# Kernel tuning notes

Hardware: AMD Instinct MI355X
Metric: run time of the kernel (lower is better)

## Reference

```python
import jax, jax.numpy as jnp
import numpy as np
from jax import lax

B, CIN, COUT, K, H, W = 16, 256, 256, 3, 128, 128
R = 16  # LoRA rank


def setup_inputs() -> dict:
    key = jax.random.key(0)
    ks = jax.random.split(key, 16)
    s = 0.05
    return {
        "x": jax.random.normal(ks[0], (B, CIN, H, W), jnp.float32),
        "wms": jax.random.normal(ks[1], (2, B, 32), jnp.float32),
        "conv_w": jax.random.normal(ks[2], (COUT, CIN, K, K), jnp.float32) * s,
        "conv_b": jax.random.normal(ks[3], (COUT,), jnp.float32) * s,
        "e1_w1": jax.random.normal(ks[4], (128, 32), jnp.float32) * s,
        "e1_b1": jax.random.normal(ks[5], (128,), jnp.float32) * s,
        "e1_w2": jax.random.normal(ks[6], (256, 128), jnp.float32) * s,
        "e1_b2": jax.random.normal(ks[7], (256,), jnp.float32) * s,
        "e2_w1": jax.random.normal(ks[8], (128, 32), jnp.float32) * s,
        "e2_b1": jax.random.normal(ks[9], (128,), jnp.float32) * s,
        "e2_w2": jax.random.normal(ks[10], (256, 128), jnp.float32) * s,
        "e2_b2": jax.random.normal(ks[11], (256,), jnp.float32) * s,
        "lora_A1": jax.random.normal(ks[12], (R, CIN * K), jnp.float32),
        "lora_A2": jax.random.normal(ks[13], (R, CIN * K), jnp.float32),
        "lora_B": jax.random.normal(ks[14], (COUT * K, R), jnp.float32) * s,
    }


def _embed(v, w1, b1, w2, b2):
    # Linear(32,128) -> LeakyReLU(0.2) -> Linear(128,256)
    h = v @ w1.T + b1
    h = jnp.where(h >= 0, h, 0.2 * h)
    return h @ w2.T + b2


def _conv_same(x, w):
    # NCHW conv, stride 1, padding 1
    return lax.conv_general_dilated(x, w, (1, 1), [(1, 1), (1, 1)],
                                    dimension_numbers=("NCHW", "OIHW", "NCHW"))


def reference(x, wms, conv_w, conv_b, e1_w1, e1_b1, e1_w2, e1_b2,
              e2_w1, e2_b1, e2_w2, e2_b2, lora_A1, lora_A2, lora_B):
    wm1, wm2 = wms[0], wms[1]
    coff1 = _embed(wm1, e1_w1, e1_b1, e1_w2, e1_b2).reshape(B, R, R)
    coff2 = _embed(wm2, e2_w1, e2_b1, e2_w2, e2_b2).reshape(B, R, R)

    org = _conv_same(x, conv_w) + conv_b[None, :, None, None]

    # per-sample LoRA weights: (COUT*K, R) @ (R,R) @ (R, CIN*K) -> (B, COUT, CIN, K, K)
    wA = jnp.einsum('pr,brq,qc->bpc', lora_B, coff1, lora_A1).reshape(B, COUT, CIN, K, K)
    wB = jnp.einsum('pr,brq,qc->bpc', lora_B, coff2, lora_A2).reshape(B, COUT, CIN, K, K)

    def per_sample_conv(xi, wi):
        return _conv_same(xi[None], wi)[0]

    outA = jax.vmap(per_sample_conv)(x, wA)
    outB = jax.vmap(per_sample_conv)(x, wB)
    return org + outA + outB
```

## Files before the change

### kernel.cpp

```cpp
#include <hip/hip_runtime.h>
#include <hip/hip_bf16.h>
#include <stdint.h>

typedef __bf16 bf16x8 __attribute__((ext_vector_type(8)));
typedef float f32x4 __attribute__((ext_vector_type(4)));
typedef unsigned short ushort8v __attribute__((ext_vector_type(8)));

#define NB    16
#define CIN   256
#define COUT  256
#define HH    128
#define WW    128

#define OFF_ZROW  0u
#define OFF_COFF  (1u << 16)
#define OFF_TMPS  (1u << 17)
#define OFF_WEFF  (1u << 20)
#define OFF_XT    (20u * 1024u * 1024u)
#define XT_PER_B  (128u * 128u * 256u * 2u)

__device__ inline void gload16(const void* g, void* l) {
  __builtin_amdgcn_global_load_lds(
      (const __attribute__((address_space(1))) void*)g,
      (__attribute__((address_space(3))) void*)l, 16, 0, 0);
}

__device__ inline ushort f2bf(float f) {
  __hip_bfloat16 h = __float2bfloat16(f);
  union { __hip_bfloat16 b; ushort u; } cv;
  cv.b = h;
  return cv.u;
}

__global__ void k_coff(const float* __restrict__ wms,
                       const float* __restrict__ w1a, const float* __restrict__ b1a,
                       const float* __restrict__ w2a, const float* __restrict__ b2a,
                       const float* __restrict__ w1b, const float* __restrict__ b1b,
                       const float* __restrict__ w2b, const float* __restrict__ b2b,
                       float* __restrict__ coff) {
  int br = blockIdx.x >> 4, b = blockIdx.x & 15;
  const float* w1 = br ? w1b : w1a;
  const float* b1 = br ? b1b : b1a;
  const float* w2 = br ? w2b : w2a;
  const float* b2 = br ? b2b : b2a;
  const float* v = wms + (br * 16 + b) * 32;
  __shared__ float h[128];
  int t = threadIdx.x;
  if (t < 128) {
    float a = b1[t];
#pragma unroll
    for (int i = 0; i < 32; ++i) a += w1[t * 32 + i] * v[i];
    h[t] = a >= 0.f ? a : 0.2f * a;
  }
  __syncthreads();
  float a = b2[t];
  for (int j = 0; j < 128; ++j) a += w2[t * 128 + j] * h[j];
  coff[(br * 16 + b) * 256 + t] = a;
}

__global__ void k_tmps(const float* __restrict__ coff,
                       const float* __restrict__ A1, const float* __restrict__ A2,
                       float* __restrict__ tmpS) {
  int b = blockIdx.x >> 4, r = blockIdx.x & 15;
  __shared__ float c1[16], c2[16];
  int t = threadIdx.x;
  if (t < 16) {
    c1[t] = coff[b * 256 + r * 16 + t];
    c2[t] = coff[(16 + b) * 256 + r * 16 + t];
  }
  __syncthreads();
  for (int c = t; c < 768; c += 256) {
    float s = 0.f;
#pragma unroll
    for (int q = 0; q < 16; ++q) s += c1[q] * A1[q * 768 + c] + c2[q] * A2[q * 768 + c];
    tmpS[(b * 16 + r) * 768 + c] = s;
  }
}

__global__ __launch_bounds__(256) void k_weff(const float* __restrict__ conv_w,
                                              const float* __restrict__ loraB,
                                              const float* __restrict__ tmpS,
                                              __hip_bfloat16* __restrict__ Weff) {
  int bid = blockIdx.x;
  int co = bid & 255, b = bid >> 8;
  int t = threadIdx.x;
  __shared__ float Bs[3][16];
  __shared__ ushort obuf[2304];
  if (t < 48) Bs[t >> 4][t & 15] = loraB[(co * 3 + (t >> 4)) * 16 + (t & 15)];
  __syncthreads();
  const float* T = tmpS + (size_t)b * 16 * 768;
  const float* W = conv_w + (size_t)co * 2304;
#pragma unroll
  for (int k = 0; k < 3; ++k) {
#pragma unroll
    for (int cc = 0; cc < 3; ++cc) {
      int c = cc * 256 + t;
      float s = W[k * 768 + c];
#pragma unroll
      for (int r = 0; r < 16; ++r) s += Bs[k][r] * T[r * 768 + c];
      int f = k * 768 + c;
      int ci = f / 9, tt = f - ci * 9;
      obuf[tt * 256 + ci] = f2bf(s);
    }
  }
  __syncthreads();
#pragma unroll
  for (int tt = 0; tt < 9; ++tt)
    ((ushort*)Weff)[((size_t)(b * 9 + tt) * 256 + co) * 256 + t] = obuf[tt * 256 + t];
}

__global__ __launch_bounds__(256) void k_xt(const float* __restrict__ x,
                                            __hip_bfloat16* __restrict__ xT, int b0) {
  __shared__ ushort t[32][132];
  int bid = blockIdx.x;
  int cb = bid & 7, h = (bid >> 3) & 127, bp = bid >> 10;
  int b = b0 + bp;
  int tid = threadIdx.x;
  int ci2 = tid >> 5, w4 = (tid & 31) * 4;
  const float* srcb = x + ((size_t)(b * 256 + cb * 32) * 128 + h) * 128;
#pragma unroll
  for (int k = 0; k < 4; ++k) {
    int c = ci2 + k * 8;
    float4 v = *(const float4*)(srcb + (size_t)c * 16384 + w4);
    ushort4 u;
    u.x = f2bf(v.x);
    u.y = f2bf(v.y);
    u.z = f2bf(v.z);
    u.w = f2bf(v.w);
    *(ushort4*)&t[c][w4] = u;
  }
  __syncthreads();
  int w = tid >> 1, hf = tid & 1;
  ushort8v o0, o1;
#pragma unroll
  for (int j = 0; j < 8; ++j) {
    o0[j] = t[hf * 16 + j][w];
    o1[j] = t[hf * 16 + 8 + j][w];
  }
  ushort* dst = (ushort*)xT + (size_t)bp * 128 * 128 * 256 +
                ((size_t)h * 128 + w) * 256 + cb * 32 + hf * 16;
  *(ushort8v*)dst = o0;
  *(ushort8v*)(dst + 8) = o1;
}

__global__ __launch_bounds__(512) void k_conv(
    const __hip_bfloat16* __restrict__ xT,
    const __hip_bfloat16* __restrict__ Weff,
    const __hip_bfloat16* __restrict__ zrow,
    const float* __restrict__ cbias,
    float* __restrict__ out, int b0) {
  __shared__ __align__(16) __hip_bfloat16 xs[4 * 130 * 32];
  __shared__ __align__(16) __hip_bfloat16 wbuf[3 * 256 * 32];

  int bid = blockIdx.x;
  int hp = bid & 63, bp = bid >> 6;
  int b = b0 + bp;
  int h0 = hp * 2;

  int tid = threadIdx.x;
  int wid = tid >> 6, lane = tid & 63;
  int l15 = lane & 15, lh = lane >> 4;
  int wm = wid >> 2, wn = wid & 3;
  int row = wn >> 1, w0 = (wn & 1) * 64;
  int lrow = lane >> 2;
  int sgx = (lane & 3) ^ (((1 + lrow) >> 1) & 3);
  int sgw = (lane & 3) ^ ((lrow >> 1) & 3);
  int asw = (l15 >> 1) & 3;

  if (tid < 256) {
    int ri = tid >> 6, which = (tid >> 5) & 1, ci = tid & 31;
    ((ushort*)xs)[ri * 4160 + (which ? 129 : 0) * 32 + ci] = 0;
  }

  f32x4 acc[8][4];
#pragma unroll
  for (int mf = 0; mf < 8; ++mf)
#pragma unroll
    for (int nf = 0; nf < 4; ++nf) acc[mf][nf] = (f32x4){0.f, 0.f, 0.f, 0.f};

  const __hip_bfloat16* xTb = xT + (size_t)bp * 128 * 128 * 256;

  for (int cb8 = 0; cb8 < 8; ++cb8) {
    int c0 = cb8 * 32;
    __syncthreads();

#pragma unroll
    for (int k = 0; k < 4; ++k) {
      int s = wid * 4 + k;
      int ri = s >> 3, wblk = s & 7;
      int h = h0 + ri - 1;
      const __hip_bfloat16* srow = (h >= 0 && h < 128) ? (xTb + (size_t)h * 128 * 256) : zrow;
      const __hip_bfloat16* src = srow + (wblk * 16 + lrow) * 256 + c0 + sgx * 8;
      gload16((const void*)src, (void*)(xs + ri * 4160 + (1 + wblk * 16) * 32));
    }

#pragma unroll 1
    for (int kh = 0; kh < 3; ++kh) {
      if (kh) __syncthreads();
#pragma unroll
      for (int k = 0; k < 6; ++k) {
        int s = wid * 6 + k;
        int kw = s >> 4, cblk = s & 15;
        const __hip_bfloat16* src =
            Weff + (((size_t)(b * 9 + kh * 3 + kw) * 256 + cblk * 16 + lrow) * 256 +
                    c0 + sgw * 8);
        gload16((const void*)src, (void*)(wbuf + kw * 8192 + cblk * 512));
      }
      __syncthreads();

#pragma unroll
      for (int kw = 0; kw < 3; ++kw) {
        int bsw = ((l15 + kw) >> 1) & 3;
        bf16x8 af[8], bfr[4];
#pragma unroll
        for (int mf = 0; mf < 8; ++mf)
          af[mf] = *(const bf16x8*)&wbuf[kw * 8192 + (wm * 128 + mf * 16 + l15) * 32 +
                                         ((lh ^ asw) * 8)];
#pragma unroll
        for (int nf = 0; nf < 4; ++nf)
          bfr[nf] = *(const bf16x8*)&xs[(row + kh) * 4160 +
                                        (w0 + nf * 16 + l15 + kw) * 32 + ((lh ^ bsw) * 8)];
#pragma unroll
        for (int mf = 0; mf < 8; ++mf)
#pragma unroll
          for (int nf = 0; nf < 4; ++nf)
            acc[mf][nf] = __builtin_amdgcn_mfma_f32_16x16x32_bf16(af[mf], bfr[nf], acc[mf][nf], 0, 0, 0);
      }
    }
  }

#pragma unroll
  for (int mf = 0; mf < 8; ++mf) {
    int cobase = wm * 128 + mf * 16 + lh * 4;
#pragma unroll
    for (int r = 0; r < 4; ++r) {
      int co = cobase + r;
      float bias = cbias[co];
      size_t obase = ((size_t)(b * 256 + co) * 128 + (h0 + row)) * 128 + w0 + l15;
#pragma unroll
      for (int nf = 0; nf < 4; ++nf) out[obase + nf * 16] = acc[mf][nf][r] + bias;
    }
  }
}

extern "C" void kernel_launch(void* const* d_in, const int* in_sizes, int n_in,
                              void* d_out, int out_size, void* d_ws, size_t ws_size,
                              hipStream_t stream) {
  const float* x      = (const float*)d_in[0];
  const float* wms    = (const float*)d_in[1];
  const float* conv_w = (const float*)d_in[2];
  const float* conv_b = (const float*)d_in[3];
  const float* e1w1   = (const float*)d_in[4];
  const float* e1b1   = (const float*)d_in[5];
  const float* e1w2   = (const float*)d_in[6];
  const float* e1b2   = (const float*)d_in[7];
  const float* e2w1   = (const float*)d_in[8];
  const float* e2b1   = (const float*)d_in[9];
  const float* e2w2   = (const float*)d_in[10];
  const float* e2b2   = (const float*)d_in[11];
  const float* A1     = (const float*)d_in[12];
  const float* A2     = (const float*)d_in[13];
  const float* loraB  = (const float*)d_in[14];
  float* out = (float*)d_out;

  uint8_t* ws = (uint8_t*)d_ws;
  __hip_bfloat16* zrow = (__hip_bfloat16*)(ws + OFF_ZROW);
  float* coff          = (float*)(ws + OFF_COFF);
  float* tmpS          = (float*)(ws + OFF_TMPS);
  __hip_bfloat16* Weff = (__hip_bfloat16*)(ws + OFF_WEFF);
  __hip_bfloat16* xT   = (__hip_bfloat16*)(ws + OFF_XT);

  int G = 16;
  while (G > 1 && (size_t)OFF_XT + (size_t)G * XT_PER_B > ws_size) G >>= 1;

  hipMemsetAsync(zrow, 0, 65536, stream);
  k_coff<<<32, 256, 0, stream>>>(wms, e1w1, e1b1, e1w2, e1b2, e2w1, e2b1, e2w2, e2b2, coff);
  k_tmps<<<256, 256, 0, stream>>>(coff, A1, A2, tmpS);
  k_weff<<<16 * 256, 256, 0, stream>>>(conv_w, loraB, tmpS, Weff);
  for (int g = 0; g < 16; g += G) {
    k_xt<<<G * 1024, 256, 0, stream>>>(x, xT, g);
    k_conv<<<G * 64, 512, 0, stream>>>(xT, Weff, zrow, conv_b, out, g);
  }
}
```

Before: 486.7 us.

## Double-buffer conv weight and input tiles, switch to 32x32x16 MFMA

Restructures the implicit-GEMM conv main loop. Weight slices are now loaded one tap at a time into a double buffer and the next channel block of input rows is prefetched into a second buffer, so global-to-LDS loads overlap with MFMA work instead of stalling behind a barrier. The inner product moves from 16x16x32 to 32x32x16 MFMA with a matching swizzle and epilogue, and the code adds s_setprio around the math plus a two-blocks-per-CU occupancy hint. The cost is doubled LDS for the input tile, one barrier per tap, and more register pressure under the tighter launch bound.

New measurement: 514.1 us. 5.6% more time.

```diff
diff --git a/kernel.cpp b/kernel.cpp
--- a/kernel.cpp
+++ b/kernel.cpp
@@ -3,7 +3,7 @@
 #include <stdint.h>
 
 typedef __bf16 bf16x8 __attribute__((ext_vector_type(8)));
-typedef float f32x4 __attribute__((ext_vector_type(4)));
+typedef float f32x16 __attribute__((ext_vector_type(16)));
 typedef unsigned short ushort8v __attribute__((ext_vector_type(8)));
 
 #define NB    16
@@ -143,14 +143,14 @@
   *(ushort8v*)(dst + 8) = o1;
 }
 
-__global__ __launch_bounds__(512) void k_conv(
+__global__ __launch_bounds__(512, 2) void k_conv(
     const __hip_bfloat16* __restrict__ xT,
     const __hip_bfloat16* __restrict__ Weff,
     const __hip_bfloat16* __restrict__ zrow,
     const float* __restrict__ cbias,
     float* __restrict__ out, int b0) {
-  __shared__ __align__(16) __hip_bfloat16 xs[4 * 130 * 32];
-  __shared__ __align__(16) __hip_bfloat16 wbuf[3 * 256 * 32];
+  __shared__ __align__(16) __hip_bfloat16 xs[2 * 4 * 130 * 32];
+  __shared__ __align__(16) __hip_bfloat16 wsl[2 * 256 * 32];
 
   int bid = blockIdx.x;
   int hp = bid & 63, bp = bid >> 6;
@@ -159,86 +159,133 @@
 
   int tid = threadIdx.x;
   int wid = tid >> 6, lane = tid & 63;
-  int l15 = lane & 15, lh = lane >> 4;
+  int l31 = lane & 31, gh = lane >> 5;
   int wm = wid >> 2, wn = wid & 3;
   int row = wn >> 1, w0 = (wn & 1) * 64;
   int lrow = lane >> 2;
   int sgx = (lane & 3) ^ (((1 + lrow) >> 1) & 3);
   int sgw = (lane & 3) ^ ((lrow >> 1) & 3);
-  int asw = (l15 >> 1) & 3;
-
-  if (tid < 256) {
-    int ri = tid >> 6, which = (tid >> 5) & 1, ci = tid & 31;
-    ((ushort*)xs)[ri * 4160 + (which ? 129 : 0) * 32 + ci] = 0;
-  }
-
-  f32x4 acc[8][4];
-#pragma unroll
-  for (int mf = 0; mf < 8; ++mf)
-#pragma unroll
-    for (int nf = 0; nf < 4; ++nf) acc[mf][nf] = (f32x4){0.f, 0.f, 0.f, 0.f};
+  int x2 = (l31 >> 1) & 3;
+
+  ((ushort*)xs)[(tid >> 8) * 16640 + ((tid >> 6) & 3) * 4160 +
+                (((tid >> 5) & 1) ? 129 * 32 : 0) + (tid & 31)] = 0;
 
   const __hip_bfloat16* xTb = xT + (size_t)bp * 128 * 128 * 256;
 
-  for (int cb8 = 0; cb8 < 8; ++cb8) {
-    int c0 = cb8 * 32;
-    __syncthreads();
-
+  {
+    int cblk = wid * 2;
+#pragma unroll
+    for (int k = 0; k < 2; ++k)
+      gload16(Weff + (((size_t)(b * 9 + 0) * 256 + (cblk + k) * 16 + lrow) * 256 + sgw * 8),
+              wsl + (cblk + k) * 512);
 #pragma unroll
     for (int k = 0; k < 4; ++k) {
       int s = wid * 4 + k;
       int ri = s >> 3, wblk = s & 7;
       int h = h0 + ri - 1;
       const __hip_bfloat16* srow = (h >= 0 && h < 128) ? (xTb + (size_t)h * 128 * 256) : zrow;
-      const __hip_bfloat16* src = srow + (wblk * 16 + lrow) * 256 + c0 + sgx * 8;
-      gload16((const void*)src, (void*)(xs + ri * 4160 + (1 + wblk * 16) * 32));
+      gload16(srow + (wblk * 16 + lrow) * 256 + sgx * 8,
+              xs + ri * 4160 + (1 + wblk * 16) * 32);
     }
+  }
+
+  f32x16 acc[4][2];
+#pragma unroll
+  for (int mf = 0; mf < 4; ++mf)
+#pragma unroll
+    for (int nf = 0; nf < 2; ++nf)
+#pragma unroll
+      for (int q = 0; q < 16; ++q) acc[mf][nf][q] = 0.f;
+
+  __syncthreads();
 
 #pragma unroll 1
+  for (int cb8 = 0; cb8 < 8; ++cb8) {
+    const __hip_bfloat16* xsb = xs + (cb8 & 1) * 16640;
+#pragma unroll
     for (int kh = 0; kh < 3; ++kh) {
-      if (kh) __syncthreads();
-#pragma unroll
-      for (int k = 0; k < 6; ++k) {
-        int s = wid * 6 + k;
-        int kw = s >> 4, cblk = s & 15;
-        const __hip_bfloat16* src =
-            Weff + (((size_t)(b * 9 + kh * 3 + kw) * 256 + cblk * 16 + lrow) * 256 +
-                    c0 + sgw * 8);
-        gload16((const void*)src, (void*)(wbuf + kw * 8192 + cblk * 512));
-      }
-      __syncthreads();
-
 #pragma unroll
       for (int kw = 0; kw < 3; ++kw) {
-        int bsw = ((l15 + kw) >> 1) & 3;
-        bf16x8 af[8], bfr[4];
-#pragma unroll
-        for (int mf = 0; mf < 8; ++mf)
-          af[mf] = *(const bf16x8*)&wbuf[kw * 8192 + (wm * 128 + mf * 16 + l15) * 32 +
-                                         ((lh ^ asw) * 8)];
-#pragma unroll
-        for (int nf = 0; nf < 4; ++nf)
-          bfr[nf] = *(const bf16x8*)&xs[(row + kh) * 4160 +
-                                        (w0 + nf * 16 + l15 + kw) * 32 + ((lh ^ bsw) * 8)];
-#pragma unroll
-        for (int mf = 0; mf < 8; ++mf)
-#pragma unroll
-          for (int nf = 0; nf < 4; ++nf)
-            acc[mf][nf] = __builtin_amdgcn_mfma_f32_16x16x32_bf16(af[mf], bfr[nf], acc[mf][nf], 0, 0, 0);
+        const int tap = kh * 3 + kw;
+        int cur = (cb8 ^ tap) & 1;
+        const __hip_bfloat16* wcur = wsl + cur * 8192;
+        __hip_bfloat16* wnxt = wsl + (cur ^ 1) * 8192;
+
+        if (tap < 8) {
+          int cblk = wid * 2;
+#pragma unroll
+          for (int k = 0; k < 2; ++k)
+            gload16(Weff + (((size_t)(b * 9 + tap + 1) * 256 + (cblk + k) * 16 + lrow) * 256 +
+                            cb8 * 32 + sgw * 8),
+                    wnxt + (cblk + k) * 512);
+        } else if (cb8 < 7) {
+          int cblk = wid * 2;
+#pragma unroll
+          for (int k = 0; k < 2; ++k)
+            gload16(Weff + (((size_t)(b * 9 + 0) * 256 + (cblk + k) * 16 + lrow) * 256 +
+                            (cb8 + 1) * 32 + sgw * 8),
+                    wnxt + (cblk + k) * 512);
+        }
+        if (tap == 0 && cb8 < 7) {
+          __hip_bfloat16* xnxt = xs + ((cb8 + 1) & 1) * 16640;
+          int c0n = (cb8 + 1) * 32;
+#pragma unroll
+          for (int k = 0; k < 4; ++k) {
+            int s = wid * 4 + k;
+            int ri = s >> 3, wblk = s & 7;
+            int h = h0 + ri - 1;
+            const __hip_bfloat16* srow = (h >= 0 && h < 128) ? (xTb + (size_t)h * 128 * 256) : zrow;
+            gload16(srow + (wblk * 16 + lrow) * 256 + c0n + sgx * 8,
+                    xnxt + ri * 4160 + (1 + wblk * 16) * 32);
+          }
+        }
+
+        bf16x8 a[4][2], bb[2][2];
+#pragma unroll
+        for (int mf = 0; mf < 4; ++mf) {
+          int r = wm * 128 + mf * 32 + l31;
+#pragma unroll
+          for (int kk = 0; kk < 2; ++kk)
+            a[mf][kk] = *(const bf16x8*)&wcur[r * 32 + (((kk * 2 + gh) ^ x2) * 8)];
+        }
+#pragma unroll
+        for (int nf = 0; nf < 2; ++nf) {
+          int wi = w0 + nf * 32 + l31 + kw;
+          int swz = (wi >> 1) & 3;
+          int rbase = (row + kh) * 4160 + wi * 32;
+#pragma unroll
+          for (int kk = 0; kk < 2; ++kk)
+            bb[nf][kk] = *(const bf16x8*)&xsb[rbase + (((kk * 2 + gh) ^ swz) * 8)];
+        }
+
+        __builtin_amdgcn_s_setprio(1);
+#pragma unroll
+        for (int kk = 0; kk < 2; ++kk)
+#pragma unroll
+          for (int mf = 0; mf < 4; ++mf)
+#pragma unroll
+            for (int nf = 0; nf < 2; ++nf)
+              acc[mf][nf] = __builtin_amdgcn_mfma_f32_32x32x16_bf16(a[mf][kk], bb[nf][kk],
+                                                                    acc[mf][nf], 0, 0, 0);
+        __builtin_amdgcn_s_setprio(0);
+        __syncthreads();
       }
     }
   }
 
 #pragma unroll
-  for (int mf = 0; mf < 8; ++mf) {
-    int cobase = wm * 128 + mf * 16 + lh * 4;
-#pragma unroll
-    for (int r = 0; r < 4; ++r) {
-      int co = cobase + r;
-      float bias = cbias[co];
-      size_t obase = ((size_t)(b * 256 + co) * 128 + (h0 + row)) * 128 + w0 + l15;
-#pragma unroll
-      for (int nf = 0; nf < 4; ++nf) out[obase + nf * 16] = acc[mf][nf][r] + bias;
+  for (int mf = 0; mf < 4; ++mf) {
+#pragma unroll
+    for (int rg = 0; rg < 4; ++rg) {
+#pragma unroll
+      for (int rr = 0; rr < 4; ++rr) {
+        int reg = rg * 4 + rr;
+        int co = wm * 128 + mf * 32 + rr + rg * 8 + gh * 4;
+        float bias = cbias[co];
+        size_t obase = ((size_t)(b * 256 + co) * 128 + (h0 + row)) * 128 + w0 + l31;
+        out[obase] = acc[mf][0][reg] + bias;
+        out[obase + 32] = acc[mf][1][reg] + bias;
+      }
     }
   }
 }
```

## Pipeline conv weight taps and input slabs with triple/double-buffered async loads

Applied to the files above, without the earlier changes.

Restructures the conv main loop so weights are streamed one tap at a time into a three-slot ring, prefetched two taps ahead, and input channel slabs are double-buffered and prefetched one channel group ahead. Full __syncthreads are replaced with vmcnt-based waits plus raw barriers, and MFMA sections get raised wave priority. The aim is to hide global-to-LDS load latency behind MFMA work instead of stalling at each kh step. It doubles the xs LDS footprint and depends on hand-counted vmcnt values, which could break correctness if miscounted.

New measurement: 561.8 us. +15.5%, slower.

```diff
diff --git a/kernel.cpp b/kernel.cpp
--- a/kernel.cpp
+++ b/kernel.cpp
@@ -18,6 +18,8 @@
 #define OFF_WEFF  (1u << 20)
 #define OFF_XT    (20u * 1024u * 1024u)
 #define XT_PER_B  (128u * 128u * 256u * 2u)
+
+#define WAITVM(N) asm volatile("s_waitcnt vmcnt(" #N ")" ::: "memory")
 
 __device__ inline void gload16(const void* g, void* l) {
   __builtin_amdgcn_global_load_lds(
@@ -149,8 +151,8 @@
     const __hip_bfloat16* __restrict__ zrow,
     const float* __restrict__ cbias,
     float* __restrict__ out, int b0) {
-  __shared__ __align__(16) __hip_bfloat16 xs[4 * 130 * 32];
-  __shared__ __align__(16) __hip_bfloat16 wbuf[3 * 256 * 32];
+  __shared__ __align__(16) __hip_bfloat16 xs[2 * 4 * 130 * 32];
+  __shared__ __align__(16) __hip_bfloat16 wsl[3 * 256 * 32];
 
   int bid = blockIdx.x;
   int hp = bid & 63, bp = bid >> 6;
@@ -167,64 +169,110 @@
   int sgw = (lane & 3) ^ ((lrow >> 1) & 3);
   int asw = (l15 >> 1) & 3;
 
-  if (tid < 256) {
-    int ri = tid >> 6, which = (tid >> 5) & 1, ci = tid & 31;
-    ((ushort*)xs)[ri * 4160 + (which ? 129 : 0) * 32 + ci] = 0;
-  }
-
-  f32x4 acc[8][4];
-#pragma unroll
-  for (int mf = 0; mf < 8; ++mf)
-#pragma unroll
-    for (int nf = 0; nf < 4; ++nf) acc[mf][nf] = (f32x4){0.f, 0.f, 0.f, 0.f};
+  ((ushort*)xs)[(tid >> 8) * 16640 + ((tid >> 6) & 3) * 4160 +
+                (((tid >> 5) & 1) ? 129 * 32 : 0) + (tid & 31)] = 0;
 
   const __hip_bfloat16* xTb = xT + (size_t)bp * 128 * 128 * 256;
 
-  for (int cb8 = 0; cb8 < 8; ++cb8) {
-    int c0 = cb8 * 32;
-    __syncthreads();
-
+  {
 #pragma unroll
     for (int k = 0; k < 4; ++k) {
       int s = wid * 4 + k;
       int ri = s >> 3, wblk = s & 7;
       int h = h0 + ri - 1;
       const __hip_bfloat16* srow = (h >= 0 && h < 128) ? (xTb + (size_t)h * 128 * 256) : zrow;
-      const __hip_bfloat16* src = srow + (wblk * 16 + lrow) * 256 + c0 + sgx * 8;
-      gload16((const void*)src, (void*)(xs + ri * 4160 + (1 + wblk * 16) * 32));
+      gload16(srow + (wblk * 16 + lrow) * 256 + sgx * 8,
+              xs + ri * 4160 + (1 + wblk * 16) * 32);
     }
+    int cblk = wid * 2;
+#pragma unroll
+    for (int st = 0; st < 2; ++st)
+#pragma unroll
+      for (int k = 0; k < 2; ++k)
+        gload16(Weff + (((size_t)(b * 9 + st) * 256 + (cblk + k) * 16 + lrow) * 256 + sgw * 8),
+                wsl + st * 8192 + (cblk + k) * 512);
+  }
+
+  f32x4 acc[8][4];
+#pragma unroll
+  for (int mf = 0; mf < 8; ++mf)
+#pragma unroll
+    for (int nf = 0; nf < 4; ++nf) acc[mf][nf] = (f32x4){0.f, 0.f, 0.f, 0.f};
+
+  asm volatile("s_waitcnt vmcnt(2) lgkmcnt(0)" ::: "memory");
+  __builtin_amdgcn_s_barrier();
 
 #pragma unroll 1
+  for (int g = 0; g < 8; ++g) {
+    const __hip_bfloat16* xsb = xs + (g & 1) * 16640;
+#pragma unroll
     for (int kh = 0; kh < 3; ++kh) {
-      if (kh) __syncthreads();
-#pragma unroll
-      for (int k = 0; k < 6; ++k) {
-        int s = wid * 6 + k;
-        int kw = s >> 4, cblk = s & 15;
-        const __hip_bfloat16* src =
-            Weff + (((size_t)(b * 9 + kh * 3 + kw) * 256 + cblk * 16 + lrow) * 256 +
-                    c0 + sgw * 8);
-        gload16((const void*)src, (void*)(wbuf + kw * 8192 + cblk * 512));
-      }
-      __syncthreads();
-
 #pragma unroll
       for (int kw = 0; kw < 3; ++kw) {
+        const int t = kh * 3 + kw;
+        const int slot = t % 3;
+        const __hip_bfloat16* wcur = wsl + slot * 8192;
+
+        if (g < 7 || t < 7) {
+          const int tap2 = (t + 2) % 9;
+          int g2 = g + (t + 2) / 9;
+          int cblk = wid * 2;
+#pragma unroll
+          for (int k = 0; k < 2; ++k)
+            gload16(Weff + (((size_t)(b * 9 + tap2) * 256 + (cblk + k) * 16 + lrow) * 256 +
+                            g2 * 32 + sgw * 8),
+                    wsl + ((t + 2) % 3) * 8192 + (cblk + k) * 512);
+        }
+        if (t == 0 && g < 7) {
+          __hip_bfloat16* xnxt = xs + ((g + 1) & 1) * 16640;
+          int c0n = (g + 1) * 32;
+#pragma unroll
+          for (int k = 0; k < 4; ++k) {
+            int s = wid * 4 + k;
+            int ri = s >> 3, wblk = s & 7;
+            int h = h0 + ri - 1;
+            const __hip_bfloat16* srow = (h >= 0 && h < 128) ? (xTb + (size_t)h * 128 * 256) : zrow;
+            gload16(srow + (wblk * 16 + lrow) * 256 + c0n + sgx * 8,
+                    xnxt + ri * 4160 + (1 + wblk * 16) * 32);
+          }
+        }
+
         int bsw = ((l15 + kw) >> 1) & 3;
         bf16x8 af[8], bfr[4];
 #pragma unroll
         for (int mf = 0; mf < 8; ++mf)
-          af[mf] = *(const bf16x8*)&wbuf[kw * 8192 + (wm * 128 + mf * 16 + l15) * 32 +
-                                         ((lh ^ asw) * 8)];
+          af[mf] = *(const bf16x8*)&wcur[(wm * 128 + mf * 16 + l15) * 32 + ((lh ^ asw) * 8)];
 #pragma unroll
         for (int nf = 0; nf < 4; ++nf)
-          bfr[nf] = *(const bf16x8*)&xs[(row + kh) * 4160 +
-                                        (w0 + nf * 16 + l15 + kw) * 32 + ((lh ^ bsw) * 8)];
+          bfr[nf] = *(const bf16x8*)&xsb[(row + kh) * 4160 +
+                                         (w0 + nf * 16 + l15 + kw) * 32 + ((lh ^ bsw) * 8)];
+
+        __builtin_amdgcn_s_setprio(1);
 #pragma unroll
         for (int mf = 0; mf < 8; ++mf)
 #pragma unroll
           for (int nf = 0; nf < 4; ++nf)
-            acc[mf][nf] = __builtin_amdgcn_mfma_f32_16x16x32_bf16(af[mf], bfr[nf], acc[mf][nf], 0, 0, 0);
+            acc[mf][nf] = __builtin_amdgcn_mfma_f32_16x16x32_bf16(af[mf], bfr[nf],
+                                                                  acc[mf][nf], 0, 0, 0);
+        __builtin_amdgcn_s_setprio(0);
+
+        if (g == 7) {
+          if (t < 7) {
+            WAITVM(2);
+            __builtin_amdgcn_s_barrier();
+          } else if (t == 7) {
+            WAITVM(0);
+            __builtin_amdgcn_s_barrier();
+          }
+        } else {
+          if (t < 2) {
+            WAITVM(6);
+            __builtin_amdgcn_s_barrier();
+          } else {
+            WAITVM(2);
+            __builtin_amdgcn_s_barrier();
+          }
+        }
       }
     }
   }
```

## Double-buffer weight tiles to overlap loads with MFMA, remap blocks across XCDs

Applied to the files above, without the earlier changes.

Doubles the LDS weight buffer so the next kh/channel-block weight tile is fetched with global_load_lds while MFMAs run on the current one. Plain syncthreads are replaced by explicit vmcnt waits plus s_barrier. MFMA sections are wrapped in s_setprio, and the block index is permuted so neighbouring rows land on the same XCD. The x tile is still loaded serially at each channel-block boundary with two barriers. The larger LDS footprint may reduce occupancy.

After: 553.8 us. 13.8% more time.

```diff
diff --git a/kernel.cpp b/kernel.cpp
--- a/kernel.cpp
+++ b/kernel.cpp
@@ -18,6 +18,8 @@
 #define OFF_WEFF  (1u << 20)
 #define OFF_XT    (20u * 1024u * 1024u)
 #define XT_PER_B  (128u * 128u * 256u * 2u)
+
+#define WAITVM0() asm volatile("s_waitcnt vmcnt(0)" ::: "memory")
 
 __device__ inline void gload16(const void* g, void* l) {
   __builtin_amdgcn_global_load_lds(
@@ -150,9 +152,12 @@
     const float* __restrict__ cbias,
     float* __restrict__ out, int b0) {
   __shared__ __align__(16) __hip_bfloat16 xs[4 * 130 * 32];
-  __shared__ __align__(16) __hip_bfloat16 wbuf[3 * 256 * 32];
-
-  int bid = blockIdx.x;
+  __shared__ __align__(16) __hip_bfloat16 wbuf[2 * 3 * 256 * 32];
+
+  int nwg = gridDim.x;
+  int bid0 = blockIdx.x;
+  int bid = (bid0 & 7) * (nwg >> 3) + (bid0 >> 3);
+
   int hp = bid & 63, bp = bid >> 6;
   int b = b0 + bp;
   int h0 = hp * 2;
@@ -172,41 +177,57 @@
     ((ushort*)xs)[ri * 4160 + (which ? 129 : 0) * 32 + ci] = 0;
   }
 
-  f32x4 acc[8][4];
-#pragma unroll
-  for (int mf = 0; mf < 8; ++mf)
-#pragma unroll
-    for (int nf = 0; nf < 4; ++nf) acc[mf][nf] = (f32x4){0.f, 0.f, 0.f, 0.f};
-
   const __hip_bfloat16* xTb = xT + (size_t)bp * 128 * 128 * 256;
 
-  for (int cb8 = 0; cb8 < 8; ++cb8) {
-    int c0 = cb8 * 32;
-    __syncthreads();
-
+  {
 #pragma unroll
     for (int k = 0; k < 4; ++k) {
       int s = wid * 4 + k;
       int ri = s >> 3, wblk = s & 7;
       int h = h0 + ri - 1;
       const __hip_bfloat16* srow = (h >= 0 && h < 128) ? (xTb + (size_t)h * 128 * 256) : zrow;
-      const __hip_bfloat16* src = srow + (wblk * 16 + lrow) * 256 + c0 + sgx * 8;
-      gload16((const void*)src, (void*)(xs + ri * 4160 + (1 + wblk * 16) * 32));
-    }
+      gload16(srow + (wblk * 16 + lrow) * 256 + sgx * 8,
+              xs + ri * 4160 + (1 + wblk * 16) * 32);
+    }
+#pragma unroll
+    for (int k = 0; k < 6; ++k) {
+      int s = wid * 6 + k;
+      int kw = s >> 4, cblk = s & 15;
+      gload16(Weff + (((size_t)(b * 9 + kw) * 256 + cblk * 16 + lrow) * 256 + sgw * 8),
+              wbuf + kw * 8192 + cblk * 512);
+    }
+  }
+
+  f32x4 acc[8][4];
+#pragma unroll
+  for (int mf = 0; mf < 8; ++mf)
+#pragma unroll
+    for (int nf = 0; nf < 4; ++nf) acc[mf][nf] = (f32x4){0.f, 0.f, 0.f, 0.f};
+
+  __syncthreads();
 
 #pragma unroll 1
+  for (int g = 0; g < 8; ++g) {
+    int c0 = g * 32;
+#pragma unroll
     for (int kh = 0; kh < 3; ++kh) {
-      if (kh) __syncthreads();
-#pragma unroll
-      for (int k = 0; k < 6; ++k) {
-        int s = wid * 6 + k;
-        int kw = s >> 4, cblk = s & 15;
-        const __hip_bfloat16* src =
-            Weff + (((size_t)(b * 9 + kh * 3 + kw) * 256 + cblk * 16 + lrow) * 256 +
-                    c0 + sgw * 8);
-        gload16((const void*)src, (void*)(wbuf + kw * 8192 + cblk * 512));
+      const int p = g * 3 + kh;
+      const __hip_bfloat16* wcur = wbuf + (p & 1) * 24576;
+      __hip_bfloat16* wnxt = wbuf + ((p + 1) & 1) * 24576;
+
+      if (g < 7 || kh < 2) {
+        const int khn = (kh + 1) % 3;
+        int tapbase = b * 9 + khn * 3;
+        int c0n = (kh < 2) ? c0 : c0 + 32;
+#pragma unroll
+        for (int k = 0; k < 6; ++k) {
+          int s = wid * 6 + k;
+          int kw = s >> 4, cblk = s & 15;
+          gload16(Weff + (((size_t)(tapbase + kw) * 256 + cblk * 16 + lrow) * 256 +
+                          c0n + sgw * 8),
+                  wnxt + kw * 8192 + cblk * 512);
+        }
       }
-      __syncthreads();
 
 #pragma unroll
       for (int kw = 0; kw < 3; ++kw) {
@@ -214,17 +235,40 @@
         bf16x8 af[8], bfr[4];
 #pragma unroll
         for (int mf = 0; mf < 8; ++mf)
-          af[mf] = *(const bf16x8*)&wbuf[kw * 8192 + (wm * 128 + mf * 16 + l15) * 32 +
+          af[mf] = *(const bf16x8*)&wcur[kw * 8192 + (wm * 128 + mf * 16 + l15) * 32 +
                                          ((lh ^ asw) * 8)];
 #pragma unroll
         for (int nf = 0; nf < 4; ++nf)
           bfr[nf] = *(const bf16x8*)&xs[(row + kh) * 4160 +
                                         (w0 + nf * 16 + l15 + kw) * 32 + ((lh ^ bsw) * 8)];
+        __builtin_amdgcn_s_setprio(1);
 #pragma unroll
         for (int mf = 0; mf < 8; ++mf)
 #pragma unroll
           for (int nf = 0; nf < 4; ++nf)
-            acc[mf][nf] = __builtin_amdgcn_mfma_f32_16x16x32_bf16(af[mf], bfr[nf], acc[mf][nf], 0, 0, 0);
+            acc[mf][nf] = __builtin_amdgcn_mfma_f32_16x16x32_bf16(af[mf], bfr[nf],
+                                                                  acc[mf][nf], 0, 0, 0);
+        __builtin_amdgcn_s_setprio(0);
+      }
+
+      if (kh < 2) {
+        WAITVM0();
+        __builtin_amdgcn_s_barrier();
+      } else if (g < 7) {
+        WAITVM0();
+        __builtin_amdgcn_s_barrier();
+        int c0n = (g + 1) * 32;
+#pragma unroll
+        for (int k = 0; k < 4; ++k) {
+          int s = wid * 4 + k;
+          int ri = s >> 3, wblk = s & 7;
+          int h = h0 + ri - 1;
+          const __hip_bfloat16* srow = (h >= 0 && h < 128) ? (xTb + (size_t)h * 128 * 256) : zrow;
+          gload16(srow + (wblk * 16 + lrow) * 256 + c0n + sgx * 8,
+                  xs + ri * 4160 + (1 + wblk * 16) * 32);
+        }
+        WAITVM0();
+        __builtin_amdgcn_s_barrier();
       }
     }
   }
```
